# Kernel tuning notes

Hardware: AMD Instinct MI355X
Metric: run time of the kernel (lower is better)

The kernel has to match this reference:

```python
import jax, jax.numpy as jnp
import numpy as np

EPS_LN = 1e-6  # ieps_ln_default


def setup_inputs() -> dict:
    key = jax.random.key(0)
    ks = jax.random.split(key, 8)
    B, S, H, ID = 8, 2048, 8, 256  # batch, seq, heads, i_head_dim
    OD = 256                        # o_head_dim
    sc_hid = 1.0 / np.sqrt(2 * ID)
    sc_og = 1.0 / np.sqrt(ID + OD)
    return {
        "heads_input": jax.random.normal(ks[0], (B, S, H, ID), dtype=jnp.float32),
        "W_hid": jax.random.uniform(ks[1], (3 * OD, 2 * ID), jnp.float32, -sc_hid, sc_hid),
        "b_hid": jnp.zeros((3 * OD,), jnp.float32),
        "W_og": jax.random.uniform(ks[2], (OD, ID + OD), jnp.float32, -sc_og, sc_og),
        "b_og": jnp.zeros((OD,), jnp.float32),
        "ln_w": jnp.ones((H, ID), jnp.float32),
        "ln_b": jnp.zeros((H, ID), jnp.float32),
        "init_cx": jnp.zeros((H, OD), jnp.float32),
    }


def _forward(heads_input, W_hid, b_hid, W_og, b_og, ln_w, ln_b, init_cx):
    B, S, H, ID = heads_input.shape
    OD = init_cx.shape[-1]
    # RS1cumsumstatnorm: causal running sum, LayerNorm over (heads, dim) jointly
    csum = jnp.cumsum(heads_input, axis=1)
    mean = jnp.mean(csum, axis=(-2, -1), keepdims=True)
    var = jnp.var(csum, axis=(-2, -1), keepdims=True)
    csum = (csum - mean) * jax.lax.rsqrt(var + EPS_LN) * ln_w + ln_b
    # trans_hid on cat(input, csum): [B,S,H,2*ID] -> [B,S,H,3*OD]
    x2 = jnp.concatenate([heads_input, csum], axis=-1)
    g = jnp.einsum('bshd,od->bsho', x2, W_hid) + b_hid
    g = g.reshape(B, S, H, 3, OD)
    igate, fgate, hidden = g[..., 0, :], g[..., 1, :], g[..., 2, :]
    fgate = jax.nn.sigmoid(fgate)
    igh = jax.nn.sigmoid(igate) * jax.nn.relu(hidden)
    # LGateFunc: cell_t = f_t * cell_{t-1} + igh_t, starting from init_cx
    c0 = jnp.broadcast_to(init_cx, (B, H, OD))

    def step(c, fi):
        f, ig = fi
        c = f * c + ig
        return c, c

    _, cells = jax.lax.scan(step, c0, (jnp.moveaxis(fgate, 1, 0), jnp.moveaxis(igh, 1, 0)))
    cell = jnp.moveaxis(cells, 0, 1)  # [B,S,H,OD]
    # output gate on cat(input, cell)
    xo = jnp.concatenate([heads_input, cell], axis=-1)
    og = jax.nn.sigmoid(jnp.einsum('bshd,od->bsho', xo, W_og) + b_og)
    return og * cell


def reference(heads_input, W_hid, b_hid, W_og, b_og, ln_w, ln_b, init_cx):
    return _forward(heads_input, W_hid, b_hid, W_og, b_og, ln_w, ln_b, init_cx)
```

## Files before the change

### kernel.cpp

```cpp
#include <hip/hip_runtime.h>

typedef unsigned short u16;
typedef unsigned int u32;

typedef __attribute__((ext_vector_type(8))) short bf16x8;
typedef __attribute__((ext_vector_type(4))) float f32x4;

#define B_ 8
#define S_ 2048
#define H_ 8
#define ID_ 256
#define OD_ 256
#define K_ 512
#define M_ (B_*S_*H_)
#define N1_ 768
#define N2_ 256
#define G2_ 512

#define CSCH 64
#define CSST (S_/CSCH)

#define OFF_X2   (0ull)
#define SZ_X2    ((unsigned long long)M_*K_*2)
#define OFF_G    (OFF_X2 + SZ_X2)
#define SZ_G     ((unsigned long long)M_*G2_*2)
#define OFF_WH   (OFF_G + SZ_G)
#define SZ_WH    ((unsigned long long)N1_*K_*2)
#define OFF_WO   (OFF_WH + SZ_WH)
#define SZ_WO    ((unsigned long long)N2_*K_*2)
#define OFF_AUX  (OFF_WO + SZ_WO)
#define SZ_AUX   ((unsigned long long)B_*CSCH*2048*4)
#define OFF_CF   (OFF_AUX + SZ_AUX)
#define SZ_CARR  ((unsigned long long)B_*H_*32*256*4)
#define OFF_CC   (OFF_CF + SZ_CARR)
#define OFF_CIN  (OFF_CC + SZ_CARR)

__device__ __forceinline__ u16 f2bf(float f) {
    union { float f; u32 u; } v; v.f = f;
    u32 u = v.u;
    u += 0x7fffu + ((u >> 16) & 1u);
    return (u16)(u >> 16);
}
__device__ __forceinline__ float bf2f(u16 h) {
    union { u32 u; float f; } v; v.u = ((u32)h) << 16;
    return v.f;
}
__device__ __forceinline__ u32 pack2h(float a, float b) {
    union { _Float16 h; u16 u; } x, y;
    x.h = (_Float16)a; y.h = (_Float16)b;
    return (u32)x.u | ((u32)y.u << 16);
}
__device__ __forceinline__ float h2f(u16 u) {
    union { u16 u; _Float16 h; } v; v.u = u;
    return (float)v.h;
}
__device__ __forceinline__ float sigm(float x) {
    return 1.0f / (1.0f + __expf(-x));
}

__device__ __forceinline__ void gld16(const void* g, void* l) {
    __builtin_amdgcn_global_load_lds(
        (const __attribute__((address_space(1))) void*)g,
        (__attribute__((address_space(3))) void*)l, 16, 0, 0);
}

__device__ __forceinline__ int whid_src_row(int n) {
    const int t = n >> 7, c = n & 127;
    if (t < 4) {
        const int wn = (c >> 6) & 1, jj = (c & 63) >> 4, l = c & 15;
        const int o = t * 64 + wn * 32 + (jj & 1) * 16 + l;
        return (jj < 2) ? o : (512 + o);
    }
    return 256 + (t - 4) * 128 + c;
}

__global__ __launch_bounds__(256) void wconv_kernel(
    const float* __restrict__ Whid, const float* __restrict__ Wog,
    u16* __restrict__ WhB, u16* __restrict__ WoB)
{
    int idx = blockIdx.x * 256 + threadIdx.x;
    if (idx < N1_*K_) {
        const int n = idx >> 9, k = idx & 511;
        WhB[idx] = f2bf(Whid[(size_t)whid_src_row(n) * K_ + k]);
    }
    if (idx < N2_*K_) WoB[idx] = f2bf(Wog[idx]);
}

__global__ __launch_bounds__(256) void csum_phase1(
    const float* __restrict__ X, float* __restrict__ aux)
{
    const int bch = blockIdx.x;
    const int b = bch / CSCH, ch = bch % CSCH;
    const int t = threadIdx.x;
    float acc[8];
#pragma unroll
    for (int h = 0; h < 8; ++h) acc[h] = 0.f;
    for (int i = 0; i < CSST; ++i) {
        const int s = ch * CSST + i;
        const float* xp = X + ((size_t)(b * S_ + s)) * 2048 + t;
#pragma unroll
        for (int h = 0; h < 8; ++h) acc[h] += xp[h * 256];
    }
    float* ap = aux + (size_t)bch * 2048 + t;
#pragma unroll
    for (int h = 0; h < 8; ++h) ap[h * 256] = acc[h];
}

__global__ __launch_bounds__(256) void csum_mid(float* __restrict__ aux)
{
    const int idx = blockIdx.x * 256 + threadIdx.x;
    const int b = idx >> 11, c = idx & 2047;
    float run = 0.f;
    for (int ch = 0; ch < CSCH; ++ch) {
        float* p = aux + ((size_t)(b * CSCH + ch)) * 2048 + c;
        float v = *p; *p = run; run += v;
    }
}

__global__ __launch_bounds__(256) void csum_phase2(
    const float* __restrict__ X, const float* __restrict__ aux,
    const float* __restrict__ lnw, const float* __restrict__ lnb,
    u16* __restrict__ x2)
{
    const int bch = blockIdx.x;
    const int b = bch / CSCH, ch = bch % CSCH;
    const int t = threadIdx.x;
    float c[8], wv[8], bv[8];
#pragma unroll
    for (int h = 0; h < 8; ++h) {
        c[h]  = aux[(size_t)bch * 2048 + h * 256 + t];
        wv[h] = lnw[h * 256 + t];
        bv[h] = lnb[h * 256 + t];
    }
    __shared__ float red[2][4];
    for (int i = 0; i < CSST; ++i) {
        const int s = ch * CSST + i;
        const float* xp = X + ((size_t)(b * S_ + s)) * 2048 + t;
        float xa[8];
#pragma unroll
        for (int h = 0; h < 8; ++h) { xa[h] = xp[h * 256]; c[h] += xa[h]; }
        float sx = 0.f, sq = 0.f;
#pragma unroll
        for (int h = 0; h < 8; ++h) { sx += c[h]; sq += c[h] * c[h]; }
#pragma unroll
        for (int off = 32; off >= 1; off >>= 1) {
            sx += __shfl_down(sx, (unsigned)off);
            sq += __shfl_down(sq, (unsigned)off);
        }
        const int wid = t >> 6;
        if ((t & 63) == 0) { red[0][wid] = sx; red[1][wid] = sq; }
        __syncthreads();
        const float tsx = red[0][0] + red[0][1] + red[0][2] + red[0][3];
        const float tsq = red[1][0] + red[1][1] + red[1][2] + red[1][3];
        __syncthreads();
        const float mean = tsx * (1.f / 2048.f);
        const float var  = tsq * (1.f / 2048.f) - mean * mean;
        const float rstd = rsqrtf(var + 1e-6f);
        const size_t mrow = ((size_t)(b * S_ + s)) * H_;
#pragma unroll
        for (int h = 0; h < 8; ++h) {
            u16* row = x2 + (mrow + h) * (size_t)K_;
            row[t]       = f2bf(xa[h]);
            row[256 + t] = f2bf((c[h] - mean) * rstd * wv[h] + bv[h]);
        }
    }
}

template<int N, int EPI>
__global__ __launch_bounds__(256) void gemm_kernel(
    const u16* __restrict__ A, const u16* __restrict__ Bw,
    u16* __restrict__ Gout, const float* __restrict__ bias,
    const u16* __restrict__ cellbuf, float* __restrict__ Out)
{
    constexpr int NT = N / 128;
    const int blk = blockIdx.x;
    const int xcd = blk & 7;
    const int j = blk >> 3;
    const int tileN = j % NT;
    const int tileM = (j / NT) * 8 + xcd;
    const int m0 = tileM * 128, n0 = tileN * 128;
    const int tid = threadIdx.x;
    const int lane = tid & 63;
    const int w = tid >> 6, wm = w & 1, wn = w >> 1;
    const int l15 = lane & 15, quad = lane >> 4;

    __shared__ __align__(16) u16 smem[2 * 128 * 64];
    u16* As = smem;
    u16* Bs = smem + 128 * 64;

    const int lane3 = lane >> 3;
    const int pc = lane & 7;
    const int ra7 = l15 & 7;

    f32x4 acc[4][4];
    const f32x4 zero4 = {0.f, 0.f, 0.f, 0.f};
#pragma unroll
    for (int i = 0; i < 4; ++i)
#pragma unroll
        for (int jj = 0; jj < 4; ++jj) acc[i][jj] = zero4;

    for (int kt = 0; kt < K_ / 64; ++kt) {
        const int k0 = kt * 64;
#pragma unroll
        for (int p = 0; p < 4; ++p) {
            const int R0 = w * 32 + p * 8;
            const int r = R0 + lane3;
            const int ca = (pc ^ (r & 7)) * 8;
            gld16(A  + (size_t)(m0 + r) * K_ + k0 + ca, As + R0 * 64);
            gld16(Bw + (size_t)(n0 + r) * K_ + k0 + ca, Bs + R0 * 64);
        }
        asm volatile("s_waitcnt vmcnt(0)" ::: "memory");
        __syncthreads();
#pragma unroll
        for (int kk = 0; kk < 2; ++kk) {
            bf16x8 af[4], bfr[4];
#pragma unroll
            for (int i = 0; i < 4; ++i) {
                const int rowa = wm * 64 + i * 16 + l15;
                const int rowb = wn * 64 + i * 16 + l15;
                const int ca = ((kk * 4 + quad) ^ ra7) * 8;
                af[i]  = *(const bf16x8*)(const void*)(&As[rowa * 64 + ca]);
                bfr[i] = *(const bf16x8*)(const void*)(&Bs[rowb * 64 + ca]);
            }
#pragma unroll
            for (int i = 0; i < 4; ++i)
#pragma unroll
                for (int jj = 0; jj < 4; ++jj)
                    acc[i][jj] = __builtin_amdgcn_mfma_f32_16x16x32_bf16(
                        af[i], bfr[jj], acc[i][jj], 0, 0, 0);
        }
        __syncthreads();
    }

    if (EPI == 0) {
        const int m_base = m0 + wm * 64 + quad * 4;
        if (tileN < 4) {
            const int o0 = tileN * 64 + wn * 32 + l15;
            const float bI0 = bias[o0],        bI1 = bias[o0 + 16];
            const float bH0 = bias[512 + o0],  bH1 = bias[512 + o0 + 16];
            const int q = (tileN * 2 + wn) * 16 + l15;
#pragma unroll
            for (int i = 0; i < 4; ++i) {
#pragma unroll
                for (int r = 0; r < 4; ++r) {
                    const int m = m_base + i * 16 + r;
                    const float ig0 = sigm(acc[i][0][r] + bI0) * fmaxf(acc[i][2][r] + bH0, 0.f);
                    const float ig1 = sigm(acc[i][1][r] + bI1) * fmaxf(acc[i][3][r] + bH1, 0.f);
                    *(u32*)(void*)(Gout + (size_t)m * G2_ + 2 * q) = pack2h(ig0, ig1);
                }
            }
        } else {
            const int o0 = (tileN - 4) * 128 + wn * 64 + l15;
            const float bF0 = bias[256 + o0],      bF1 = bias[256 + o0 + 16];
            const float bF2 = bias[256 + o0 + 32], bF3 = bias[256 + o0 + 48];
            const int qA = ((tileN - 4) * 4 + wn * 2) * 16 + l15;
            const int qB = qA + 16;
#pragma unroll
            for (int i = 0; i < 4; ++i) {
#pragma unroll
                for (int r = 0; r < 4; ++r) {
                    const int m = m_base + i * 16 + r;
                    u16* row = Gout + (size_t)m * G2_ + 256;
                    *(u32*)(void*)(row + 2 * qA) =
                        pack2h(sigm(acc[i][0][r] + bF0), sigm(acc[i][1][r] + bF1));
                    *(u32*)(void*)(row + 2 * qB) =
                        pack2h(sigm(acc[i][2][r] + bF2), sigm(acc[i][3][r] + bF3));
                }
            }
        }
    } else {
        float* Cf = (float*)smem;
        const int col4 = (tid & 31) * 4;
        float4 b4 = *(const float4*)(const void*)(bias + n0 + col4);
#pragma unroll
        for (int half = 0; half < 2; ++half) {
            if (wm == half) {
#pragma unroll
                for (int i = 0; i < 4; ++i) {
                    const int lrow0 = i * 16 + quad * 4;
#pragma unroll
                    for (int jj = 0; jj < 4; ++jj) {
                        const int col = wn * 64 + jj * 16 + l15;
#pragma unroll
                        for (int r = 0; r < 4; ++r)
                            Cf[(lrow0 + r) * 128 + col] = acc[i][jj][r];
                    }
                }
            }
            __syncthreads();
#pragma unroll
            for (int q = 0; q < 8; ++q) {
                const int lrow = q * 8 + (tid >> 5);
                const int grow = m0 + half * 64 + lrow;
                float4 v = *(const float4*)(const void*)(&Cf[lrow * 128 + col4]);
                const u16* cp = cellbuf + (size_t)grow * K_ + 256 + n0 + col4;
                float4 o;
                o.x = sigm(v.x + b4.x) * bf2f(cp[0]);
                o.y = sigm(v.y + b4.y) * bf2f(cp[1]);
                o.z = sigm(v.z + b4.z) * bf2f(cp[2]);
                o.w = sigm(v.w + b4.w) * bf2f(cp[3]);
                *(float4*)(void*)(Out + (size_t)grow * N2_ + n0 + col4) = o;
            }
            __syncthreads();
        }
    }
}

__global__ __launch_bounds__(256) void scan_phase1(
    const u16* __restrict__ g2, float* __restrict__ cF, float* __restrict__ cC)
{
    const int blk = blockIdx.x;
    const int chp = blk & 7, bh = blk >> 3;
    const int h = bh & 7, b = bh >> 3;
    const int t = threadIdx.x;
    const int ch = chp * 4 + (t >> 6);
    const int o = (t & 63) * 4;
    float F[4] = {1.f, 1.f, 1.f, 1.f};
    float c[4] = {0.f, 0.f, 0.f, 0.f};
    for (int i = 0; i < 64; ++i) {
        const int s = ch * 64 + i;
        const size_t m = ((size_t)(b * S_ + s)) * H_ + h;
        const u16* gp = g2 + m * G2_;
        const uint2 igp = *(const uint2*)(const void*)(gp + o);
        const uint2 fgp = *(const uint2*)(const void*)(gp + 256 + o);
        const float f0 = h2f((u16)fgp.x), f1 = h2f((u16)(fgp.x >> 16));
        const float f2 = h2f((u16)fgp.y), f3 = h2f((u16)(fgp.y >> 16));
        c[0] = f0 * c[0] + h2f((u16)igp.x);         F[0] *= f0;
        c[1] = f1 * c[1] + h2f((u16)(igp.x >> 16)); F[1] *= f1;
        c[2] = f2 * c[2] + h2f((u16)igp.y);         F[2] *= f2;
        c[3] = f3 * c[3] + h2f((u16)(igp.y >> 16)); F[3] *= f3;
    }
    const size_t idx = ((size_t)(bh * 32 + ch)) * 256 + o;
    *(float4*)(void*)(cF + idx) = make_float4(F[0], F[1], F[2], F[3]);
    *(float4*)(void*)(cC + idx) = make_float4(c[0], c[1], c[2], c[3]);
}

__global__ __launch_bounds__(256) void scan_mid(
    const float* __restrict__ cF, const float* __restrict__ cC,
    const float* __restrict__ initcx, float* __restrict__ cin)
{
    const int bh = blockIdx.x;
    const int h = bh & 7;
    const int a = threadIdx.x;
    const int q = a >> 1, hfl = a & 1;
    const int ro = ((q >> 4) << 5) + (q & 15) + (hfl << 4);
    float c = initcx[h * 256 + ro];
    for (int ch = 0; ch < 32; ++ch) {
        const size_t idx = ((size_t)(bh * 32 + ch)) * 256 + a;
        cin[idx] = c;
        c = cF[idx] * c + cC[idx];
    }
}

__global__ __launch_bounds__(256) void scan_phase2(
    const u16* __restrict__ g2, const float* __restrict__ cin,
    u16* __restrict__ x2)
{
    const int blk = blockIdx.x;
    const int chp = blk & 7, bh = blk >> 3;
    const int h = bh & 7, b = bh >> 3;
    const int t = threadIdx.x;
    const int ch = chp * 4 + (t >> 6);
    const int z = t & 63;
    const int o = z * 4;
    const int oA = ((z >> 3) << 5) + ((z & 7) << 1);
    const size_t idx = ((size_t)(bh * 32 + ch)) * 256 + o;
    float4 c4 = *(const float4*)(const void*)(cin + idx);
    float c[4] = {c4.x, c4.y, c4.z, c4.w};
    for (int i = 0; i < 64; ++i) {
        const int s = ch * 64 + i;
        const size_t m = ((size_t)(b * S_ + s)) * H_ + h;
        const u16* gp = g2 + m * G2_;
        const uint2 igp = *(const uint2*)(const void*)(gp + o);
        const uint2 fgp = *(const uint2*)(const void*)(gp + 256 + o);
        const float f0 = h2f((u16)fgp.x), f1 = h2f((u16)(fgp.x >> 16));
        const float f2 = h2f((u16)fgp.y), f3 = h2f((u16)(fgp.y >> 16));
        c[0] = f0 * c[0] + h2f((u16)igp.x);
        c[1] = f1 * c[1] + h2f((u16)(igp.x >> 16));
        c[2] = f2 * c[2] + h2f((u16)igp.y);
        c[3] = f3 * c[3] + h2f((u16)(igp.y >> 16));
        u16* xr = x2 + m * K_ + 256;
        const u32 pkA = (u32)f2bf(c[0]) | ((u32)f2bf(c[2]) << 16);
        const u32 pkB = (u32)f2bf(c[1]) | ((u32)f2bf(c[3]) << 16);
        *(u32*)(void*)(xr + oA)      = pkA;
        *(u32*)(void*)(xr + oA + 16) = pkB;
    }
}

extern "C" void kernel_launch(void* const* d_in, const int* in_sizes, int n_in,
                              void* d_out, int out_size, void* d_ws, size_t ws_size,
                              hipStream_t stream)
{
    const float* X      = (const float*)d_in[0];
    const float* Whid   = (const float*)d_in[1];
    const float* bhid   = (const float*)d_in[2];
    const float* Wog    = (const float*)d_in[3];
    const float* bog    = (const float*)d_in[4];
    const float* lnw    = (const float*)d_in[5];
    const float* lnb    = (const float*)d_in[6];
    const float* initcx = (const float*)d_in[7];
    float* out = (float*)d_out;

    char* ws = (char*)d_ws;
    u16* x2   = (u16*)(ws + OFF_X2);
    u16* g    = (u16*)(ws + OFF_G);
    u16* WhB  = (u16*)(ws + OFF_WH);
    u16* WoB  = (u16*)(ws + OFF_WO);
    float* aux = (float*)(ws + OFF_AUX);
    float* cF  = (float*)(ws + OFF_CF);
    float* cC  = (float*)(ws + OFF_CC);
    float* cin = (float*)(ws + OFF_CIN);

    wconv_kernel<<<(N1_*K_ + 255) / 256, 256, 0, stream>>>(Whid, Wog, WhB, WoB);
    csum_phase1<<<B_ * CSCH, 256, 0, stream>>>(X, aux);
    csum_mid<<<64, 256, 0, stream>>>(aux);
    csum_phase2<<<B_ * CSCH, 256, 0, stream>>>(X, aux, lnw, lnb, x2);
    gemm_kernel<N1_, 0><<<(M_ / 128) * (N1_ / 128), 256, 0, stream>>>(
        x2, WhB, g, bhid, nullptr, nullptr);
    scan_phase1<<<B_ * H_ * 8, 256, 0, stream>>>(g, cF, cC);
    scan_mid<<<B_ * H_, 256, 0, stream>>>(cF, cC, initcx, cin);
    scan_phase2<<<B_ * H_ * 8, 256, 0, stream>>>(g, cin, x2);
    gemm_kernel<N2_, 1><<<(M_ / 128) * (N2_ / 128), 256, 0, stream>>>(
        x2, WoB, nullptr, bog, x2, out);
}
```

Baseline: 623.4 us.

## Restructure GEMM to 256x256 tiles with 4-stage async LDS pipeline

Both GEMMs now use 256x256 output tiles with 512 threads (8 waves), BK=32 and a four-buffer LDS ring. Global-to-LDS loads are issued three stages ahead, with vmcnt-gated barriers, so memory latency overlaps the MFMA work. The Whid row permutation and the epilogue indexing are remapped to the new wave layout. The second GEMM's epilogue now writes directly from registers with strided scalar stores instead of staging through LDS. The larger tiles raise reuse per loaded byte, at the cost of higher register pressure, 128KB of LDS per block, and less coalesced output stores.

```diff
diff --git a/kernel.cpp b/kernel.cpp
--- a/kernel.cpp
+++ b/kernel.cpp
@@ -65,13 +65,13 @@
 }
 
 __device__ __forceinline__ int whid_src_row(int n) {
-    const int t = n >> 7, c = n & 127;
-    if (t < 4) {
-        const int wn = (c >> 6) & 1, jj = (c & 63) >> 4, l = c & 15;
-        const int o = t * 64 + wn * 32 + (jj & 1) * 16 + l;
+    const int t = n >> 8, c = n & 255;
+    if (t < 2) {
+        const int wn = c >> 6, jj = (c >> 4) & 3, l = c & 15;
+        const int o = t * 128 + wn * 32 + (jj & 1) * 16 + l;
         return (jj < 2) ? o : (512 + o);
     }
-    return 256 + (t - 4) * 128 + c;
+    return 256 + (n - 512);
 }
 
 __global__ __launch_bounds__(256) void wconv_kernel(
@@ -167,141 +167,137 @@
 }
 
 template<int N, int EPI>
-__global__ __launch_bounds__(256) void gemm_kernel(
+__global__ __launch_bounds__(512, 2) void gemm_kernel(
     const u16* __restrict__ A, const u16* __restrict__ Bw,
     u16* __restrict__ Gout, const float* __restrict__ bias,
     const u16* __restrict__ cellbuf, float* __restrict__ Out)
 {
-    constexpr int NT = N / 128;
+    constexpr int NT = N / 256;
+    constexpr int KT = K_ / 32;
     const int blk = blockIdx.x;
     const int xcd = blk & 7;
     const int j = blk >> 3;
     const int tileN = j % NT;
     const int tileM = (j / NT) * 8 + xcd;
-    const int m0 = tileM * 128, n0 = tileN * 128;
+    const int m0 = tileM * 256, n0 = tileN * 256;
     const int tid = threadIdx.x;
     const int lane = tid & 63;
-    const int w = tid >> 6, wm = w & 1, wn = w >> 1;
+    const int w = tid >> 6;
+    const int wm = w >> 2, wn = w & 3;
     const int l15 = lane & 15, quad = lane >> 4;
 
-    __shared__ __align__(16) u16 smem[2 * 128 * 64];
-    u16* As = smem;
-    u16* Bs = smem + 128 * 64;
-
-    const int lane3 = lane >> 3;
-    const int pc = lane & 7;
-    const int ra7 = l15 & 7;
-
-    f32x4 acc[4][4];
+    __shared__ __align__(16) u16 smem[4 * 16384];
+
+    const int srow   = lane >> 2;
+    const int schunk = ((lane & 3) ^ ((lane >> 3) & 3)) * 8;
+    const u16* gA0 = A  + (size_t)(m0 + w * 32      + srow) * K_ + schunk;
+    const u16* gA1 = A  + (size_t)(m0 + w * 32 + 16 + srow) * K_ + schunk;
+    const u16* gB0 = Bw + (size_t)(n0 + w * 32      + srow) * K_ + schunk;
+    const u16* gB1 = Bw + (size_t)(n0 + w * 32 + 16 + srow) * K_ + schunk;
+
+    auto STAGE = [&](int bufb, int kt) {
+        u16* sb = smem + bufb * 16384;
+        gld16(gA0 + kt * 32, sb + (w * 32) * 32);
+        gld16(gA1 + kt * 32, sb + (w * 32 + 16) * 32);
+        gld16(gB0 + kt * 32, sb + 8192 + (w * 32) * 32);
+        gld16(gB1 + kt * 32, sb + 8192 + (w * 32 + 16) * 32);
+    };
+
+    const int swz  = (quad ^ ((l15 >> 1) & 3)) * 8;
+    const int aoff = (wm * 128 + l15) * 32 + swz;
+    const int boff = 8192 + (wn * 64 + l15) * 32 + swz;
+
+    f32x4 acc[8][4];
     const f32x4 zero4 = {0.f, 0.f, 0.f, 0.f};
 #pragma unroll
-    for (int i = 0; i < 4; ++i)
-#pragma unroll
-        for (int jj = 0; jj < 4; ++jj) acc[i][jj] = zero4;
-
-    for (int kt = 0; kt < K_ / 64; ++kt) {
-        const int k0 = kt * 64;
-#pragma unroll
-        for (int p = 0; p < 4; ++p) {
-            const int R0 = w * 32 + p * 8;
-            const int r = R0 + lane3;
-            const int ca = (pc ^ (r & 7)) * 8;
-            gld16(A  + (size_t)(m0 + r) * K_ + k0 + ca, As + R0 * 64);
-            gld16(Bw + (size_t)(n0 + r) * K_ + k0 + ca, Bs + R0 * 64);
+    for (int mi = 0; mi < 8; ++mi)
+#pragma unroll
+        for (int jj = 0; jj < 4; ++jj) acc[mi][jj] = zero4;
+
+    STAGE(0, 0); STAGE(1, 1); STAGE(2, 2);
+    asm volatile("s_waitcnt vmcnt(8)\n\ts_barrier" ::: "memory");
+
+#pragma unroll
+    for (int kt = 0; kt < KT; ++kt) {
+        const int cur = kt & 3;
+        if (kt + 3 < KT) STAGE((kt + 3) & 3, kt + 3);
+        const u16* sb = smem + cur * 16384;
+        bf16x8 af[8], bfr[4];
+#pragma unroll
+        for (int mi = 0; mi < 8; ++mi)
+            af[mi] = *(const bf16x8*)(const void*)(&sb[aoff + mi * 512]);
+#pragma unroll
+        for (int jj = 0; jj < 4; ++jj)
+            bfr[jj] = *(const bf16x8*)(const void*)(&sb[boff + jj * 512]);
+        __builtin_amdgcn_s_setprio(1);
+#pragma unroll
+        for (int mi = 0; mi < 8; ++mi)
+#pragma unroll
+            for (int jj = 0; jj < 4; ++jj)
+                acc[mi][jj] = __builtin_amdgcn_mfma_f32_16x16x32_bf16(
+                    af[mi], bfr[jj], acc[mi][jj], 0, 0, 0);
+        __builtin_amdgcn_s_setprio(0);
+        if (kt + 1 < KT) {
+            if (kt + 3 < KT)
+                asm volatile("s_waitcnt vmcnt(8) lgkmcnt(0)\n\ts_barrier" ::: "memory");
+            else if (kt + 2 < KT)
+                asm volatile("s_waitcnt vmcnt(4) lgkmcnt(0)\n\ts_barrier" ::: "memory");
+            else
+                asm volatile("s_waitcnt vmcnt(0) lgkmcnt(0)\n\ts_barrier" ::: "memory");
         }
-        asm volatile("s_waitcnt vmcnt(0)" ::: "memory");
-        __syncthreads();
-#pragma unroll
-        for (int kk = 0; kk < 2; ++kk) {
-            bf16x8 af[4], bfr[4];
-#pragma unroll
-            for (int i = 0; i < 4; ++i) {
-                const int rowa = wm * 64 + i * 16 + l15;
-                const int rowb = wn * 64 + i * 16 + l15;
-                const int ca = ((kk * 4 + quad) ^ ra7) * 8;
-                af[i]  = *(const bf16x8*)(const void*)(&As[rowa * 64 + ca]);
-                bfr[i] = *(const bf16x8*)(const void*)(&Bs[rowb * 64 + ca]);
-            }
-#pragma unroll
-            for (int i = 0; i < 4; ++i)
-#pragma unroll
-                for (int jj = 0; jj < 4; ++jj)
-                    acc[i][jj] = __builtin_amdgcn_mfma_f32_16x16x32_bf16(
-                        af[i], bfr[jj], acc[i][jj], 0, 0, 0);
-        }
-        __syncthreads();
-    }
-
+    }
+
+    const int m_base = m0 + wm * 128 + quad * 4;
     if (EPI == 0) {
-        const int m_base = m0 + wm * 64 + quad * 4;
-        if (tileN < 4) {
-            const int o0 = tileN * 64 + wn * 32 + l15;
-            const float bI0 = bias[o0],        bI1 = bias[o0 + 16];
-            const float bH0 = bias[512 + o0],  bH1 = bias[512 + o0 + 16];
-            const int q = (tileN * 2 + wn) * 16 + l15;
-#pragma unroll
-            for (int i = 0; i < 4; ++i) {
+        if (tileN < 2) {
+            const int o0 = tileN * 128 + wn * 32 + l15;
+            const float bI0 = bias[o0],            bI1 = bias[o0 + 16];
+            const float bH0 = bias[512 + o0],      bH1 = bias[512 + o0 + 16];
+            const int q = (tileN * 4 + wn) * 16 + l15;
+#pragma unroll
+            for (int mi = 0; mi < 8; ++mi) {
 #pragma unroll
                 for (int r = 0; r < 4; ++r) {
-                    const int m = m_base + i * 16 + r;
-                    const float ig0 = sigm(acc[i][0][r] + bI0) * fmaxf(acc[i][2][r] + bH0, 0.f);
-                    const float ig1 = sigm(acc[i][1][r] + bI1) * fmaxf(acc[i][3][r] + bH1, 0.f);
+                    const int m = m_base + mi * 16 + r;
+                    const float ig0 = sigm(acc[mi][0][r] + bI0) * fmaxf(acc[mi][2][r] + bH0, 0.f);
+                    const float ig1 = sigm(acc[mi][1][r] + bI1) * fmaxf(acc[mi][3][r] + bH1, 0.f);
                     *(u32*)(void*)(Gout + (size_t)m * G2_ + 2 * q) = pack2h(ig0, ig1);
                 }
             }
         } else {
-            const int o0 = (tileN - 4) * 128 + wn * 64 + l15;
-            const float bF0 = bias[256 + o0],      bF1 = bias[256 + o0 + 16];
-            const float bF2 = bias[256 + o0 + 32], bF3 = bias[256 + o0 + 48];
-            const int qA = ((tileN - 4) * 4 + wn * 2) * 16 + l15;
-            const int qB = qA + 16;
-#pragma unroll
-            for (int i = 0; i < 4; ++i) {
+            const int o0 = wn * 64 + l15;
+            const float bF0 = bias[256 + o0],       bF1 = bias[256 + o0 + 16];
+            const float bF2 = bias[256 + o0 + 32],  bF3 = bias[256 + o0 + 48];
+            const int qA = wn * 32 + l15, qB = qA + 16;
+#pragma unroll
+            for (int mi = 0; mi < 8; ++mi) {
 #pragma unroll
                 for (int r = 0; r < 4; ++r) {
-                    const int m = m_base + i * 16 + r;
+                    const int m = m_base + mi * 16 + r;
                     u16* row = Gout + (size_t)m * G2_ + 256;
                     *(u32*)(void*)(row + 2 * qA) =
-                        pack2h(sigm(acc[i][0][r] + bF0), sigm(acc[i][1][r] + bF1));
+                        pack2h(sigm(acc[mi][0][r] + bF0), sigm(acc[mi][1][r] + bF1));
                     *(u32*)(void*)(row + 2 * qB) =
-                        pack2h(sigm(acc[i][2][r] + bF2), sigm(acc[i][3][r] + bF3));
+                        pack2h(sigm(acc[mi][2][r] + bF2), sigm(acc[mi][3][r] + bF3));
                 }
             }
         }
     } else {
-        float* Cf = (float*)smem;
-        const int col4 = (tid & 31) * 4;
-        float4 b4 = *(const float4*)(const void*)(bias + n0 + col4);
-#pragma unroll
-        for (int half = 0; half < 2; ++half) {
-            if (wm == half) {
-#pragma unroll
-                for (int i = 0; i < 4; ++i) {
-                    const int lrow0 = i * 16 + quad * 4;
-#pragma unroll
-                    for (int jj = 0; jj < 4; ++jj) {
-                        const int col = wn * 64 + jj * 16 + l15;
-#pragma unroll
-                        for (int r = 0; r < 4; ++r)
-                            Cf[(lrow0 + r) * 128 + col] = acc[i][jj][r];
-                    }
-                }
+        const int colb = wn * 64 + l15;
+        float bb[4];
+#pragma unroll
+        for (int jj = 0; jj < 4; ++jj) bb[jj] = bias[colb + jj * 16];
+#pragma unroll
+        for (int mi = 0; mi < 8; ++mi) {
+#pragma unroll
+            for (int r = 0; r < 4; ++r) {
+                const int m = m_base + mi * 16 + r;
+                const u16* cp = cellbuf + (size_t)m * K_ + 256 + colb;
+                float* op = Out + (size_t)m * N2_ + colb;
+#pragma unroll
+                for (int jj = 0; jj < 4; ++jj)
+                    op[jj * 16] = sigm(acc[mi][jj][r] + bb[jj]) * bf2f(cp[jj * 16]);
             }
-            __syncthreads();
-#pragma unroll
-            for (int q = 0; q < 8; ++q) {
-                const int lrow = q * 8 + (tid >> 5);
-                const int grow = m0 + half * 64 + lrow;
-                float4 v = *(const float4*)(const void*)(&Cf[lrow * 128 + col4]);
-                const u16* cp = cellbuf + (size_t)grow * K_ + 256 + n0 + col4;
-                float4 o;
-                o.x = sigm(v.x + b4.x) * bf2f(cp[0]);
-                o.y = sigm(v.y + b4.y) * bf2f(cp[1]);
-                o.z = sigm(v.z + b4.z) * bf2f(cp[2]);
-                o.w = sigm(v.w + b4.w) * bf2f(cp[3]);
-                *(float4*)(void*)(Out + (size_t)grow * N2_ + n0 + col4) = o;
-            }
-            __syncthreads();
         }
     }
 }
@@ -415,11 +411,11 @@
     csum_phase1<<<B_ * CSCH, 256, 0, stream>>>(X, aux);
     csum_mid<<<64, 256, 0, stream>>>(aux);
     csum_phase2<<<B_ * CSCH, 256, 0, stream>>>(X, aux, lnw, lnb, x2);
-    gemm_kernel<N1_, 0><<<(M_ / 128) * (N1_ / 128), 256, 0, stream>>>(
+    gemm_kernel<N1_, 0><<<(M_ / 256) * (N1_ / 256), 512, 0, stream>>>(
         x2, WhB, g, bhid, nullptr, nullptr);
     scan_phase1<<<B_ * H_ * 8, 256, 0, stream>>>(g, cF, cC);
     scan_mid<<<B_ * H_, 256, 0, stream>>>(cF, cC, initcx, cin);
     scan_phase2<<<B_ * H_ * 8, 256, 0, stream>>>(g, cin, x2);
-    gemm_kernel<N2_, 1><<<(M_ / 128) * (N2_ / 128), 256, 0, stream>>>(
+    gemm_kernel<N2_, 1><<<(M_ / 256) * (N2_ / 256), 512, 0, stream>>>(
         x2, WoB, nullptr, bog, x2, out);
 }
```

Result: faster. 562.3 us (-9.8%).
